# Kernel optimization log

Measured on AMD Instinct MI355X. Metric: run time of the kernel, lower is better.

The kernel has to match this reference:

```python
import jax, jax.numpy as jnp
import numpy as np
from functools import partial

I, H, O = 7, 64, 3  # input_size, hidden_layer_size, output_size
B, T = 512, 2048


def _lstm_scan(x, W_ih, W_hh, b_ih, b_hh, reverse):
    """Single-direction LSTM over [B,T,I]; returns hidden states [T,B,H]
    aligned to input time order (PyTorch gate order: i, f, g, o)."""
    Bsz = x.shape[0]
    Hh = W_hh.shape[1]
    # precompute input projections for all timesteps: [B,T,4H] -> [T,B,4H]
    xp = jnp.einsum('bti,gi->btg', x, W_ih) + b_ih + b_hh
    xp = jnp.swapaxes(xp, 0, 1)

    def step(carry, xt):
        h, c = carry
        gates = xt + h @ W_hh.T                      # [B,4H]
        i, f, g, o = jnp.split(gates, 4, axis=-1)
        i = jax.nn.sigmoid(i)
        f = jax.nn.sigmoid(f)
        g = jnp.tanh(g)
        o = jax.nn.sigmoid(o)
        c = f * c + i * g
        h = o * jnp.tanh(c)
        return (h, c), h

    h0 = jnp.zeros((Bsz, Hh), dtype=x.dtype)
    c0 = jnp.zeros((Bsz, Hh), dtype=x.dtype)
    (_, _), hs = jax.lax.scan(step, (h0, c0), xp, reverse=reverse)
    return hs  # [T,B,H], time-aligned


def setup_inputs() -> dict:
    key = jax.random.key(0)
    ks = jax.random.split(key, 12)
    s = 0.1  # ~ 1/sqrt(H) init scale
    return {
        'input_seq': jax.random.normal(ks[0], (B, T, I), dtype=jnp.float32),
        'W_ih_f': jax.random.normal(ks[1], (4 * H, I), dtype=jnp.float32) * s,
        'W_hh_f': jax.random.normal(ks[2], (4 * H, H), dtype=jnp.float32) * s,
        'b_ih_f': jax.random.normal(ks[3], (4 * H,), dtype=jnp.float32) * s,
        'b_hh_f': jax.random.normal(ks[4], (4 * H,), dtype=jnp.float32) * s,
        'W_ih_b': jax.random.normal(ks[5], (4 * H, I), dtype=jnp.float32) * s,
        'W_hh_b': jax.random.normal(ks[6], (4 * H, H), dtype=jnp.float32) * s,
        'b_ih_b': jax.random.normal(ks[7], (4 * H,), dtype=jnp.float32) * s,
        'b_hh_b': jax.random.normal(ks[8], (4 * H,), dtype=jnp.float32) * s,
        'W_lin': jax.random.normal(ks[9], (O, 2 * H), dtype=jnp.float32) * s,
        'b_lin': jax.random.normal(ks[10], (O,), dtype=jnp.float32) * s,
    }


def reference(input_seq, W_ih_f, W_hh_f, b_ih_f, b_hh_f,
              W_ih_b, W_hh_b, b_ih_b, b_hh_b, W_lin, b_lin):
    # forward direction: hidden at last timestep = hs_f[-1]
    hs_f = _lstm_scan(input_seq, W_ih_f, W_hh_f, b_ih_f, b_hh_f, reverse=False)
    # backward direction: scan reversed in time, outputs time-aligned, so
    # the value at t=T-1 is hs_b[-1] (the reverse LSTM's first computed step)
    hs_b = _lstm_scan(input_seq, W_ih_b, W_hh_b, b_ih_b, b_hh_b, reverse=True)
    last = jnp.concatenate([hs_f[-1], hs_b[-1]], axis=-1)  # [B, 2H]
    return last @ W_lin.T + b_lin  # [B, O]
```

## Files before the change

### kernel.cpp

```cpp
#include <hip/hip_runtime.h>
#include <hip/hip_bf16.h>

#define TT 2048
#define BB 512
#define HH 64
#define L2E 1.44269504088896340736f

typedef _Float16 h2 __attribute__((ext_vector_type(2)));

__device__ __forceinline__ float frcp(float x){ return __builtin_amdgcn_rcpf(x); }
__device__ __forceinline__ float fexp2(float x){ return __builtin_amdgcn_exp2f(x); }
__device__ __forceinline__ float fsig(float a){ return frcp(1.0f + __expf(-a)); }
__device__ __forceinline__ float ftanh(float a){ return 1.0f - 2.0f*frcp(__expf(2.0f*a)+1.0f); }
__device__ __forceinline__ h2 pk16(float lo, float hi){
  return __builtin_bit_cast(h2, __builtin_amdgcn_cvt_pkrtz(lo, hi));
}

__global__ void __launch_bounds__(64)
__attribute__((amdgpu_waves_per_eu(1, 1)))
lstm_fwd_kernel(
    const float* __restrict__ x, const float* __restrict__ Wih,
    const float* __restrict__ Whh, const float* __restrict__ bih,
    const float* __restrict__ bhh, float* __restrict__ hout)
{
  const int b = blockIdx.x;
  const int l = threadIdx.x;

  __shared__ float xs[TT][8];
  __shared__ int4  hlds4[HH/8];

  const float* xr = x + (size_t)b*TT*7;

  #pragma unroll 1
  for (int it = 0; it < TT/64; ++it){
    const int t = it*64 + l;
    const float* p = xr + (size_t)t*7;
    float4* dst = reinterpret_cast<float4*>(&xs[t][0]);
    dst[0] = make_float4(p[0],p[1],p[2],p[3]);
    dst[1] = make_float4(p[4],p[5],p[6],0.0f);
  }

  int wb[4][32];
  #pragma unroll
  for (int q = 0; q < 4; q++){
    const float sq = (q==2) ? (-2.0f*L2E) : (-L2E);
    const float4* wr = reinterpret_cast<const float4*>(Whh + (size_t)(q*HH + l)*HH);
    #pragma unroll
    for (int k = 0; k < 16; k++){
      float4 a = wr[k];
      h2 p0 = pk16(a.x*sq, a.y*sq);
      h2 p1 = pk16(a.z*sq, a.w*sq);
      wb[q][2*k+0] = __builtin_bit_cast(int, p0);
      wb[q][2*k+1] = __builtin_bit_cast(int, p1);
      asm volatile("" : "+v"(wb[q][2*k+0]), "+v"(wb[q][2*k+1]));
    }
    __builtin_amdgcn_sched_barrier(0);
  }

  int wi16[4][4];
  float bias[4];
  #pragma unroll
  for (int q = 0; q < 4; q++){
    const float sq = (q==2) ? (-2.0f*L2E) : (-L2E);
    const int g = q*HH + l;
    wi16[q][0] = __builtin_bit_cast(int, pk16(Wih[g*7+0]*sq, Wih[g*7+1]*sq));
    wi16[q][1] = __builtin_bit_cast(int, pk16(Wih[g*7+2]*sq, Wih[g*7+3]*sq));
    wi16[q][2] = __builtin_bit_cast(int, pk16(Wih[g*7+4]*sq, Wih[g*7+5]*sq));
    wi16[q][3] = __builtin_bit_cast(int, pk16(Wih[g*7+6]*sq, 0.0f));
    asm volatile("" : "+v"(wi16[q][0]), "+v"(wi16[q][1]),
                       "+v"(wi16[q][2]), "+v"(wi16[q][3]));
    bias[q] = (bih[g] + bhh[g])*sq;
    asm volatile("" : "+v"(bias[q]));
    __builtin_amdgcn_sched_barrier(0);
  }

  if (l < HH/8) hlds4[l] = int4{0,0,0,0};

  float h = 0.0f, c = 0.0f;

  int hw[32];
  #pragma unroll
  for (int i = 0; i < 8; i++){
    int4 v = hlds4[i];
    hw[4*i+0]=v.x; hw[4*i+1]=v.y; hw[4*i+2]=v.z; hw[4*i+3]=v.w;
  }

  #pragma unroll 1
  for (int t = 0; t < TT; ++t){
    const float4 xa = *reinterpret_cast<const float4*>(&xs[t][0]);
    const float4 xb = *reinterpret_cast<const float4*>(&xs[t][4]);
    const h2 xp0 = pk16(xa.x, xa.y);
    const h2 xp1 = pk16(xa.z, xa.w);
    const h2 xp2 = pk16(xb.x, xb.y);
    const h2 xp3 = pk16(xb.z, xb.w);

    float a0 = bias[0], a1 = bias[1], a2 = bias[2], a3 = bias[3];

    #pragma unroll
    for (int k = 0; k < 32; k++){
      const h2 hh = __builtin_bit_cast(h2, hw[k]);
      a0 = __builtin_amdgcn_fdot2(__builtin_bit_cast(h2, wb[0][k]), hh, a0, false);
      a1 = __builtin_amdgcn_fdot2(__builtin_bit_cast(h2, wb[1][k]), hh, a1, false);
      a2 = __builtin_amdgcn_fdot2(__builtin_bit_cast(h2, wb[2][k]), hh, a2, false);
      a3 = __builtin_amdgcn_fdot2(__builtin_bit_cast(h2, wb[3][k]), hh, a3, false);
    }
    #pragma unroll
    for (int p = 0; p < 4; p++){
      const h2 xp = (p==0)?xp0:(p==1)?xp1:(p==2)?xp2:xp3;
      a0 = __builtin_amdgcn_fdot2(__builtin_bit_cast(h2, wi16[0][p]), xp, a0, false);
      a1 = __builtin_amdgcn_fdot2(__builtin_bit_cast(h2, wi16[1][p]), xp, a1, false);
      a2 = __builtin_amdgcn_fdot2(__builtin_bit_cast(h2, wi16[2][p]), xp, a2, false);
      a3 = __builtin_amdgcn_fdot2(__builtin_bit_cast(h2, wi16[3][p]), xp, a3, false);
    }

    const float e0 = fexp2(a0);
    const float e1 = fexp2(a1);
    const float e2 = fexp2(a2);
    const float e3 = fexp2(a3);
    const float iv = frcp(1.0f + e0);
    const float fv = frcp(1.0f + e1);
    const float gv = 2.0f*frcp(1.0f + e2) - 1.0f;
    const float ov = frcp(1.0f + e3);

    c = fv*c + iv*gv;
    const float r  = frcp(1.0f + fexp2(c*(-2.0f*L2E)));
    h = 2.0f*ov*r - ov;

    reinterpret_cast<unsigned short*>(hlds4)[l] =
        __builtin_bit_cast(unsigned short, (_Float16)h);
    #pragma unroll
    for (int i = 0; i < 8; i++){
      int4 v = hlds4[i];
      hw[4*i+0]=v.x; hw[4*i+1]=v.y; hw[4*i+2]=v.z; hw[4*i+3]=v.w;
    }
  }
  hout[b*HH + l] = h;
}

__global__ __launch_bounds__(64, 1) void lstm_bwd_lin_kernel(
    const float* __restrict__ x,   const float* __restrict__ Wib,
    const float* __restrict__ bib, const float* __restrict__ bhb,
    const float* __restrict__ Wlin,const float* __restrict__ blin,
    const float* __restrict__ hf,  float* __restrict__ out)
{
  const int b = blockIdx.x;
  const int j = threadIdx.x;
  const float* xt = x + ((size_t)b*TT + (TT-1))*7;
  float xv[7];
  #pragma unroll
  for (int k = 0; k < 7; k++) xv[k] = xt[k];

  float g4[4];
  #pragma unroll
  for (int qq = 0; qq < 4; qq++){
    const int g = qq*HH + j;
    float a = bib[g] + bhb[g];
    #pragma unroll
    for (int k = 0; k < 7; k++) a += xv[k]*Wib[g*7+k];
    g4[qq] = a;
  }
  const float iv = fsig(g4[0]);
  const float gv = ftanh(g4[2]);
  const float ov = fsig(g4[3]);
  const float cc = iv*gv;
  const float hb = ov*ftanh(cc);
  const float hfv = hf[b*HH + j];

  float s[3];
  #pragma unroll
  for (int o = 0; o < 3; o++)
    s[o] = hfv*Wlin[o*128 + j] + hb*Wlin[o*128 + 64 + j];

  #pragma unroll
  for (int o = 0; o < 3; o++){
    float v = s[o];
    #pragma unroll
    for (int m = 32; m >= 1; m >>= 1) v += __shfl_xor(v, m, 64);
    s[o] = v;
  }
  if (j == 0){
    out[b*3+0] = s[0] + blin[0];
    out[b*3+1] = s[1] + blin[1];
    out[b*3+2] = s[2] + blin[2];
  }
}

extern "C" void kernel_launch(void* const* d_in, const int* in_sizes, int n_in,
                              void* d_out, int out_size, void* d_ws, size_t ws_size,
                              hipStream_t stream)
{
  const float* x    = (const float*)d_in[0];
  const float* Wihf = (const float*)d_in[1];
  const float* Whhf = (const float*)d_in[2];
  const float* bihf = (const float*)d_in[3];
  const float* bhhf = (const float*)d_in[4];
  const float* Wihb = (const float*)d_in[5];
  const float* bibb = (const float*)d_in[7];
  const float* bhbb = (const float*)d_in[8];
  const float* Wlin = (const float*)d_in[9];
  const float* blin = (const float*)d_in[10];
  float* out = (float*)d_out;
  float* hf  = (float*)d_ws;

  lstm_fwd_kernel<<<BB, 64, 0, stream>>>(x, Wihf, Whhf, bihf, bhhf, hf);
  lstm_bwd_lin_kernel<<<BB, 64, 0, stream>>>(x, Wihb, bibb, bhbb, Wlin, blin, hf, out);
}
```

Before: 826.2 us.

## Move g/o recurrent weights to LDS and allow two waves per EU

Keeps the i and f gate recurrent weights in registers and moves the g and o gate weights (fp16-packed) into shared memory, reloading them from LDS every timestep. This cuts VGPR use so the waves_per_eu hint can rise to 2, letting two blocks share an EU to hide the serial recurrence latency. x is also pre-packed to fp16 in LDS, so the per-step conversions disappear. The cost is 16 extra 128-bit LDS reads per step per lane, and LDS use grows to about 48KB per block, which may limit how many blocks fit per CU.

```diff
diff --git a/kernel.cpp b/kernel.cpp
--- a/kernel.cpp
+++ b/kernel.cpp
@@ -15,9 +15,13 @@
 __device__ __forceinline__ h2 pk16(float lo, float hi){
   return __builtin_bit_cast(h2, __builtin_amdgcn_cvt_pkrtz(lo, hi));
 }
+__device__ __forceinline__ float dot2(int w, int hp, float acc){
+  return __builtin_amdgcn_fdot2(__builtin_bit_cast(h2, w),
+                                __builtin_bit_cast(h2, hp), acc, false);
+}
 
 __global__ void __launch_bounds__(64)
-__attribute__((amdgpu_waves_per_eu(1, 1)))
+__attribute__((amdgpu_waves_per_eu(1, 2)))
 lstm_fwd_kernel(
     const float* __restrict__ x, const float* __restrict__ Wih,
     const float* __restrict__ Whh, const float* __restrict__ bih,
@@ -26,8 +30,9 @@
   const int b = blockIdx.x;
   const int l = threadIdx.x;
 
-  __shared__ float xs[TT][8];
-  __shared__ int4  hlds4[HH/8];
+  __shared__ int4 xsf4[TT];
+  __shared__ int4 wgo[2][8][HH];
+  __shared__ int4 hlds4[HH/8];
 
   const float* xr = x + (size_t)b*TT*7;
 
@@ -35,24 +40,49 @@
   for (int it = 0; it < TT/64; ++it){
     const int t = it*64 + l;
     const float* p = xr + (size_t)t*7;
-    float4* dst = reinterpret_cast<float4*>(&xs[t][0]);
-    dst[0] = make_float4(p[0],p[1],p[2],p[3]);
-    dst[1] = make_float4(p[4],p[5],p[6],0.0f);
-  }
-
-  int wb[4][32];
-  #pragma unroll
-  for (int q = 0; q < 4; q++){
-    const float sq = (q==2) ? (-2.0f*L2E) : (-L2E);
+    int4 v;
+    v.x = __builtin_bit_cast(int, pk16(p[0], p[1]));
+    v.y = __builtin_bit_cast(int, pk16(p[2], p[3]));
+    v.z = __builtin_bit_cast(int, pk16(p[4], p[5]));
+    v.w = __builtin_bit_cast(int, pk16(p[6], 0.0f));
+    xsf4[t] = v;
+  }
+
+  #pragma unroll
+  for (int g = 0; g < 2; ++g){
+    const int q = 2 + g;
+    const float sq = (q == 2) ? (-2.0f*L2E) : (-L2E);
     const float4* wr = reinterpret_cast<const float4*>(Whh + (size_t)(q*HH + l)*HH);
     #pragma unroll
+    for (int kb = 0; kb < 8; ++kb){
+      float4 a = wr[2*kb], b4 = wr[2*kb+1];
+      int4 v;
+      v.x = __builtin_bit_cast(int, pk16(a.x*sq,  a.y*sq));
+      v.y = __builtin_bit_cast(int, pk16(a.z*sq,  a.w*sq));
+      v.z = __builtin_bit_cast(int, pk16(b4.x*sq, b4.y*sq));
+      v.w = __builtin_bit_cast(int, pk16(b4.z*sq, b4.w*sq));
+      wgo[g][kb][l] = v;
+    }
+  }
+
+  int wbi[32], wbf[32];
+  {
+    const float4* wri = reinterpret_cast<const float4*>(Whh + (size_t)(0*HH + l)*HH);
+    const float4* wrf = reinterpret_cast<const float4*>(Whh + (size_t)(1*HH + l)*HH);
+    #pragma unroll
     for (int k = 0; k < 16; k++){
-      float4 a = wr[k];
-      h2 p0 = pk16(a.x*sq, a.y*sq);
-      h2 p1 = pk16(a.z*sq, a.w*sq);
-      wb[q][2*k+0] = __builtin_bit_cast(int, p0);
-      wb[q][2*k+1] = __builtin_bit_cast(int, p1);
-      asm volatile("" : "+v"(wb[q][2*k+0]), "+v"(wb[q][2*k+1]));
+      float4 a = wri[k];
+      wbi[2*k+0] = __builtin_bit_cast(int, pk16(a.x*(-L2E), a.y*(-L2E)));
+      wbi[2*k+1] = __builtin_bit_cast(int, pk16(a.z*(-L2E), a.w*(-L2E)));
+      asm volatile("" : "+v"(wbi[2*k+0]), "+v"(wbi[2*k+1]));
+    }
+    __builtin_amdgcn_sched_barrier(0);
+    #pragma unroll
+    for (int k = 0; k < 16; k++){
+      float4 a = wrf[k];
+      wbf[2*k+0] = __builtin_bit_cast(int, pk16(a.x*(-L2E), a.y*(-L2E)));
+      wbf[2*k+1] = __builtin_bit_cast(int, pk16(a.z*(-L2E), a.w*(-L2E)));
+      asm volatile("" : "+v"(wbf[2*k+0]), "+v"(wbf[2*k+1]));
     }
     __builtin_amdgcn_sched_barrier(0);
   }
@@ -67,11 +97,7 @@
     wi16[q][1] = __builtin_bit_cast(int, pk16(Wih[g*7+2]*sq, Wih[g*7+3]*sq));
     wi16[q][2] = __builtin_bit_cast(int, pk16(Wih[g*7+4]*sq, Wih[g*7+5]*sq));
     wi16[q][3] = __builtin_bit_cast(int, pk16(Wih[g*7+6]*sq, 0.0f));
-    asm volatile("" : "+v"(wi16[q][0]), "+v"(wi16[q][1]),
-                       "+v"(wi16[q][2]), "+v"(wi16[q][3]));
     bias[q] = (bih[g] + bhh[g])*sq;
-    asm volatile("" : "+v"(bias[q]));
-    __builtin_amdgcn_sched_barrier(0);
   }
 
   if (l < HH/8) hlds4[l] = int4{0,0,0,0};
@@ -87,31 +113,48 @@
 
   #pragma unroll 1
   for (int t = 0; t < TT; ++t){
-    const float4 xa = *reinterpret_cast<const float4*>(&xs[t][0]);
-    const float4 xb = *reinterpret_cast<const float4*>(&xs[t][4]);
-    const h2 xp0 = pk16(xa.x, xa.y);
-    const h2 xp1 = pk16(xa.z, xa.w);
-    const h2 xp2 = pk16(xb.x, xb.y);
-    const h2 xp3 = pk16(xb.z, xb.w);
+    const int4 xv = xsf4[t];
+
+    int4 g0 = wgo[0][0][l], g1 = wgo[0][1][l], g2 = wgo[0][2][l], g3 = wgo[0][3][l];
+    int4 g4 = wgo[0][4][l], g5 = wgo[0][5][l], g6 = wgo[0][6][l], g7 = wgo[0][7][l];
 
     float a0 = bias[0], a1 = bias[1], a2 = bias[2], a3 = bias[3];
 
     #pragma unroll
     for (int k = 0; k < 32; k++){
-      const h2 hh = __builtin_bit_cast(h2, hw[k]);
-      a0 = __builtin_amdgcn_fdot2(__builtin_bit_cast(h2, wb[0][k]), hh, a0, false);
-      a1 = __builtin_amdgcn_fdot2(__builtin_bit_cast(h2, wb[1][k]), hh, a1, false);
-      a2 = __builtin_amdgcn_fdot2(__builtin_bit_cast(h2, wb[2][k]), hh, a2, false);
-      a3 = __builtin_amdgcn_fdot2(__builtin_bit_cast(h2, wb[3][k]), hh, a3, false);
-    }
-    #pragma unroll
-    for (int p = 0; p < 4; p++){
-      const h2 xp = (p==0)?xp0:(p==1)?xp1:(p==2)?xp2:xp3;
-      a0 = __builtin_amdgcn_fdot2(__builtin_bit_cast(h2, wi16[0][p]), xp, a0, false);
-      a1 = __builtin_amdgcn_fdot2(__builtin_bit_cast(h2, wi16[1][p]), xp, a1, false);
-      a2 = __builtin_amdgcn_fdot2(__builtin_bit_cast(h2, wi16[2][p]), xp, a2, false);
-      a3 = __builtin_amdgcn_fdot2(__builtin_bit_cast(h2, wi16[3][p]), xp, a3, false);
-    }
+      a0 = dot2(wbi[k], hw[k], a0);
+      a1 = dot2(wbf[k], hw[k], a1);
+    }
+
+    int4 o0 = wgo[1][0][l], o1 = wgo[1][1][l], o2 = wgo[1][2][l], o3 = wgo[1][3][l];
+    int4 o4 = wgo[1][4][l], o5 = wgo[1][5][l], o6 = wgo[1][6][l], o7 = wgo[1][7][l];
+
+    #define GDOT(gg, kb) \
+      a2 = dot2((gg).x, hw[4*(kb)+0], a2); \
+      a2 = dot2((gg).y, hw[4*(kb)+1], a2); \
+      a2 = dot2((gg).z, hw[4*(kb)+2], a2); \
+      a2 = dot2((gg).w, hw[4*(kb)+3], a2);
+    GDOT(g0,0) GDOT(g1,1) GDOT(g2,2) GDOT(g3,3)
+    GDOT(g4,4) GDOT(g5,5) GDOT(g6,6) GDOT(g7,7)
+    #undef GDOT
+
+    #define ODOT(oo, kb) \
+      a3 = dot2((oo).x, hw[4*(kb)+0], a3); \
+      a3 = dot2((oo).y, hw[4*(kb)+1], a3); \
+      a3 = dot2((oo).z, hw[4*(kb)+2], a3); \
+      a3 = dot2((oo).w, hw[4*(kb)+3], a3);
+    ODOT(o0,0) ODOT(o1,1) ODOT(o2,2) ODOT(o3,3)
+    ODOT(o4,4) ODOT(o5,5) ODOT(o6,6) ODOT(o7,7)
+    #undef ODOT
+
+    a0 = dot2(wi16[0][0], xv.x, a0); a0 = dot2(wi16[0][1], xv.y, a0);
+    a0 = dot2(wi16[0][2], xv.z, a0); a0 = dot2(wi16[0][3], xv.w, a0);
+    a1 = dot2(wi16[1][0], xv.x, a1); a1 = dot2(wi16[1][1], xv.y, a1);
+    a1 = dot2(wi16[1][2], xv.z, a1); a1 = dot2(wi16[1][3], xv.w, a1);
+    a2 = dot2(wi16[2][0], xv.x, a2); a2 = dot2(wi16[2][1], xv.y, a2);
+    a2 = dot2(wi16[2][2], xv.z, a2); a2 = dot2(wi16[2][3], xv.w, a2);
+    a3 = dot2(wi16[3][0], xv.x, a3); a3 = dot2(wi16[3][1], xv.y, a3);
+    a3 = dot2(wi16[3][2], xv.z, a3); a3 = dot2(wi16[3][3], xv.w, a3);
 
     const float e0 = fexp2(a0);
     const float e1 = fexp2(a1);
@@ -123,7 +166,7 @@
     const float ov = frcp(1.0f + e3);
 
     c = fv*c + iv*gv;
-    const float r  = frcp(1.0f + fexp2(c*(-2.0f*L2E)));
+    const float r = frcp(1.0f + fexp2(c*(-2.0f*L2E)));
     h = 2.0f*ov*r - ov;
 
     reinterpret_cast<unsigned short*>(hlds4)[l] =
```

Measured after the change: 796.7 us. 3.6% less time.

## Process two batch rows per wavefront with W_hh staged in LDS

Applied to the files above, without the earlier changes.

Each 64-lane block now runs two independent batch sequences, interleaving their recurrences so one sequence's dot products and transcendentals can hide the other's latency. The recurrent weights move from registers into LDS and are reread every step, and x is pre-packed to fp16 in LDS. This halves the grid to 256 blocks, which is about one wave per CU on a 256-CU part, and adds per-step LDS weight traffic in exchange for more instruction-level parallelism per wave.

```diff
diff --git a/kernel.cpp b/kernel.cpp
--- a/kernel.cpp
+++ b/kernel.cpp
@@ -14,6 +14,13 @@
 __device__ __forceinline__ float ftanh(float a){ return 1.0f - 2.0f*frcp(__expf(2.0f*a)+1.0f); }
 __device__ __forceinline__ h2 pk16(float lo, float hi){
   return __builtin_bit_cast(h2, __builtin_amdgcn_cvt_pkrtz(lo, hi));
+}
+__device__ __forceinline__ int pk16i(float lo, float hi){
+  return __builtin_bit_cast(int, pk16(lo, hi));
+}
+__device__ __forceinline__ float dot2(int w, int hp, float acc){
+  return __builtin_amdgcn_fdot2(__builtin_bit_cast(h2, w),
+                                __builtin_bit_cast(h2, hp), acc, false);
 }
 
 __global__ void __launch_bounds__(64)
@@ -23,38 +30,43 @@
     const float* __restrict__ Whh, const float* __restrict__ bih,
     const float* __restrict__ bhh, float* __restrict__ hout)
 {
-  const int b = blockIdx.x;
-  const int l = threadIdx.x;
-
-  __shared__ float xs[TT][8];
-  __shared__ int4  hlds4[HH/8];
-
-  const float* xr = x + (size_t)b*TT*7;
+  const int b0 = blockIdx.x * 2;
+  const int l  = threadIdx.x;
+
+  __shared__ int4 xsf[2][TT];
+  __shared__ int4 wlds[4][8][HH];
+  __shared__ int4 hlds[2][HH/8];
 
   #pragma unroll 1
-  for (int it = 0; it < TT/64; ++it){
-    const int t = it*64 + l;
-    const float* p = xr + (size_t)t*7;
-    float4* dst = reinterpret_cast<float4*>(&xs[t][0]);
-    dst[0] = make_float4(p[0],p[1],p[2],p[3]);
-    dst[1] = make_float4(p[4],p[5],p[6],0.0f);
-  }
-
-  int wb[4][32];
-  #pragma unroll
-  for (int q = 0; q < 4; q++){
-    const float sq = (q==2) ? (-2.0f*L2E) : (-L2E);
+  for (int r = 0; r < 2; ++r){
+    const float* xr = x + (size_t)(b0 + r)*TT*7;
+    #pragma unroll 1
+    for (int it = 0; it < TT/64; ++it){
+      const int t = it*64 + l;
+      const float* p = xr + (size_t)t*7;
+      int4 v;
+      v.x = pk16i(p[0], p[1]);
+      v.y = pk16i(p[2], p[3]);
+      v.z = pk16i(p[4], p[5]);
+      v.w = pk16i(p[6], 0.0f);
+      xsf[r][t] = v;
+    }
+  }
+
+  #pragma unroll
+  for (int q = 0; q < 4; ++q){
+    const float sq = (q == 2) ? (-2.0f*L2E) : (-L2E);
     const float4* wr = reinterpret_cast<const float4*>(Whh + (size_t)(q*HH + l)*HH);
     #pragma unroll
-    for (int k = 0; k < 16; k++){
-      float4 a = wr[k];
-      h2 p0 = pk16(a.x*sq, a.y*sq);
-      h2 p1 = pk16(a.z*sq, a.w*sq);
-      wb[q][2*k+0] = __builtin_bit_cast(int, p0);
-      wb[q][2*k+1] = __builtin_bit_cast(int, p1);
-      asm volatile("" : "+v"(wb[q][2*k+0]), "+v"(wb[q][2*k+1]));
-    }
-    __builtin_amdgcn_sched_barrier(0);
+    for (int kb = 0; kb < 8; ++kb){
+      float4 a = wr[2*kb], b4 = wr[2*kb+1];
+      int4 v;
+      v.x = pk16i(a.x*sq,  a.y*sq);
+      v.y = pk16i(a.z*sq,  a.w*sq);
+      v.z = pk16i(b4.x*sq, b4.y*sq);
+      v.w = pk16i(b4.z*sq, b4.w*sq);
+      wlds[q][kb][l] = v;
+    }
   }
 
   int wi16[4][4];
@@ -63,78 +75,117 @@
   for (int q = 0; q < 4; q++){
     const float sq = (q==2) ? (-2.0f*L2E) : (-L2E);
     const int g = q*HH + l;
-    wi16[q][0] = __builtin_bit_cast(int, pk16(Wih[g*7+0]*sq, Wih[g*7+1]*sq));
-    wi16[q][1] = __builtin_bit_cast(int, pk16(Wih[g*7+2]*sq, Wih[g*7+3]*sq));
-    wi16[q][2] = __builtin_bit_cast(int, pk16(Wih[g*7+4]*sq, Wih[g*7+5]*sq));
-    wi16[q][3] = __builtin_bit_cast(int, pk16(Wih[g*7+6]*sq, 0.0f));
-    asm volatile("" : "+v"(wi16[q][0]), "+v"(wi16[q][1]),
-                       "+v"(wi16[q][2]), "+v"(wi16[q][3]));
+    wi16[q][0] = pk16i(Wih[g*7+0]*sq, Wih[g*7+1]*sq);
+    wi16[q][1] = pk16i(Wih[g*7+2]*sq, Wih[g*7+3]*sq);
+    wi16[q][2] = pk16i(Wih[g*7+4]*sq, Wih[g*7+5]*sq);
+    wi16[q][3] = pk16i(Wih[g*7+6]*sq, 0.0f);
     bias[q] = (bih[g] + bhh[g])*sq;
-    asm volatile("" : "+v"(bias[q]));
-    __builtin_amdgcn_sched_barrier(0);
-  }
-
-  if (l < HH/8) hlds4[l] = int4{0,0,0,0};
-
-  float h = 0.0f, c = 0.0f;
-
-  int hw[32];
+  }
+
+  {
+    int4* hf = &hlds[0][0];
+    if (l < 16) hf[l] = int4{0,0,0,0};
+  }
+
+  float h0 = 0.0f, c0 = 0.0f, h1 = 0.0f, c1 = 0.0f;
+
+  int hw0[32], hw1[32];
   #pragma unroll
   for (int i = 0; i < 8; i++){
-    int4 v = hlds4[i];
-    hw[4*i+0]=v.x; hw[4*i+1]=v.y; hw[4*i+2]=v.z; hw[4*i+3]=v.w;
-  }
+    int4 v = hlds[0][i];
+    hw0[4*i+0]=v.x; hw0[4*i+1]=v.y; hw0[4*i+2]=v.z; hw0[4*i+3]=v.w;
+  }
+  #pragma unroll
+  for (int i = 0; i < 8; i++){
+    int4 v = hlds[1][i];
+    hw1[4*i+0]=v.x; hw1[4*i+1]=v.y; hw1[4*i+2]=v.z; hw1[4*i+3]=v.w;
+  }
+  int4 xv0 = xsf[0][0];
+  int4 xv1 = xsf[1][0];
 
   #pragma unroll 1
   for (int t = 0; t < TT; ++t){
-    const float4 xa = *reinterpret_cast<const float4*>(&xs[t][0]);
-    const float4 xb = *reinterpret_cast<const float4*>(&xs[t][4]);
-    const h2 xp0 = pk16(xa.x, xa.y);
-    const h2 xp1 = pk16(xa.z, xa.w);
-    const h2 xp2 = pk16(xb.x, xb.y);
-    const h2 xp3 = pk16(xb.z, xb.w);
-
-    float a0 = bias[0], a1 = bias[1], a2 = bias[2], a3 = bias[3];
-
-    #pragma unroll
-    for (int k = 0; k < 32; k++){
-      const h2 hh = __builtin_bit_cast(h2, hw[k]);
-      a0 = __builtin_amdgcn_fdot2(__builtin_bit_cast(h2, wb[0][k]), hh, a0, false);
-      a1 = __builtin_amdgcn_fdot2(__builtin_bit_cast(h2, wb[1][k]), hh, a1, false);
-      a2 = __builtin_amdgcn_fdot2(__builtin_bit_cast(h2, wb[2][k]), hh, a2, false);
-      a3 = __builtin_amdgcn_fdot2(__builtin_bit_cast(h2, wb[3][k]), hh, a3, false);
-    }
-    #pragma unroll
-    for (int p = 0; p < 4; p++){
-      const h2 xp = (p==0)?xp0:(p==1)?xp1:(p==2)?xp2:xp3;
-      a0 = __builtin_amdgcn_fdot2(__builtin_bit_cast(h2, wi16[0][p]), xp, a0, false);
-      a1 = __builtin_amdgcn_fdot2(__builtin_bit_cast(h2, wi16[1][p]), xp, a1, false);
-      a2 = __builtin_amdgcn_fdot2(__builtin_bit_cast(h2, wi16[2][p]), xp, a2, false);
-      a3 = __builtin_amdgcn_fdot2(__builtin_bit_cast(h2, wi16[3][p]), xp, a3, false);
-    }
-
-    const float e0 = fexp2(a0);
-    const float e1 = fexp2(a1);
-    const float e2 = fexp2(a2);
-    const float e3 = fexp2(a3);
-    const float iv = frcp(1.0f + e0);
-    const float fv = frcp(1.0f + e1);
-    const float gv = 2.0f*frcp(1.0f + e2) - 1.0f;
-    const float ov = frcp(1.0f + e3);
-
-    c = fv*c + iv*gv;
-    const float r  = frcp(1.0f + fexp2(c*(-2.0f*L2E)));
-    h = 2.0f*ov*r - ov;
-
-    reinterpret_cast<unsigned short*>(hlds4)[l] =
-        __builtin_bit_cast(unsigned short, (_Float16)h);
-    #pragma unroll
-    for (int i = 0; i < 8; i++){
-      int4 v = hlds4[i];
-      hw[4*i+0]=v.x; hw[4*i+1]=v.y; hw[4*i+2]=v.z; hw[4*i+3]=v.w;
-    }
-  }
-  hout[b*HH + l] = h;
+    float a00 = bias[0], a01 = bias[1], a02 = bias[2], a03 = bias[3];
+    float a10 = bias[0], a11 = bias[1], a12 = bias[2], a13 = bias[3];
+
+    a00 = dot2(wi16[0][0], xv0.x, a00); a00 = dot2(wi16[0][1], xv0.y, a00);
+    a00 = dot2(wi16[0][2], xv0.z, a00); a00 = dot2(wi16[0][3], xv0.w, a00);
+    a01 = dot2(wi16[1][0], xv0.x, a01); a01 = dot2(wi16[1][1], xv0.y, a01);
+    a01 = dot2(wi16[1][2], xv0.z, a01); a01 = dot2(wi16[1][3], xv0.w, a01);
+    a02 = dot2(wi16[2][0], xv0.x, a02); a02 = dot2(wi16[2][1], xv0.y, a02);
+    a02 = dot2(wi16[2][2], xv0.z, a02); a02 = dot2(wi16[2][3], xv0.w, a02);
+    a03 = dot2(wi16[3][0], xv0.x, a03); a03 = dot2(wi16[3][1], xv0.y, a03);
+    a03 = dot2(wi16[3][2], xv0.z, a03); a03 = dot2(wi16[3][3], xv0.w, a03);
+
+    a10 = dot2(wi16[0][0], xv1.x, a10); a10 = dot2(wi16[0][1], xv1.y, a10);
+    a10 = dot2(wi16[0][2], xv1.z, a10); a10 = dot2(wi16[0][3], xv1.w, a10);
+    a11 = dot2(wi16[1][0], xv1.x, a11); a11 = dot2(wi16[1][1], xv1.y, a11);
+    a11 = dot2(wi16[1][2], xv1.z, a11); a11 = dot2(wi16[1][3], xv1.w, a11);
+    a12 = dot2(wi16[2][0], xv1.x, a12); a12 = dot2(wi16[2][1], xv1.y, a12);
+    a12 = dot2(wi16[2][2], xv1.z, a12); a12 = dot2(wi16[2][3], xv1.w, a12);
+    a13 = dot2(wi16[3][0], xv1.x, a13); a13 = dot2(wi16[3][1], xv1.y, a13);
+    a13 = dot2(wi16[3][2], xv1.z, a13); a13 = dot2(wi16[3][3], xv1.w, a13);
+
+    #pragma unroll
+    for (int q = 0; q < 4; ++q){
+      int4 w0 = wlds[q][0][l], w1 = wlds[q][1][l], w2 = wlds[q][2][l], w3 = wlds[q][3][l];
+      int4 w4 = wlds[q][4][l], w5 = wlds[q][5][l], w6 = wlds[q][6][l], w7 = wlds[q][7][l];
+      float s0, s1;
+      s0 = (q==0)?a00:(q==1)?a01:(q==2)?a02:a03;
+      s1 = (q==0)?a10:(q==1)?a11:(q==2)?a12:a13;
+      #define QD(w_, kb) \
+        s0 = dot2((w_).x, hw0[4*(kb)+0], s0); s0 = dot2((w_).y, hw0[4*(kb)+1], s0); \
+        s0 = dot2((w_).z, hw0[4*(kb)+2], s0); s0 = dot2((w_).w, hw0[4*(kb)+3], s0); \
+        s1 = dot2((w_).x, hw1[4*(kb)+0], s1); s1 = dot2((w_).y, hw1[4*(kb)+1], s1); \
+        s1 = dot2((w_).z, hw1[4*(kb)+2], s1); s1 = dot2((w_).w, hw1[4*(kb)+3], s1);
+      QD(w0,0) QD(w1,1) QD(w2,2) QD(w3,3) QD(w4,4) QD(w5,5) QD(w6,6) QD(w7,7)
+      #undef QD
+      if (q==0){ a00=s0; a10=s1; } else if (q==1){ a01=s0; a11=s1; }
+      else if (q==2){ a02=s0; a12=s1; } else { a03=s0; a13=s1; }
+    }
+
+    {
+      const float e0 = fexp2(a00), e1 = fexp2(a01), e2 = fexp2(a02), e3 = fexp2(a03);
+      const float iv = frcp(1.0f + e0);
+      const float fv = frcp(1.0f + e1);
+      const float gv = 2.0f*frcp(1.0f + e2) - 1.0f;
+      const float ov = frcp(1.0f + e3);
+      c0 = fv*c0 + iv*gv;
+      const float r = frcp(1.0f + fexp2(c0*(-2.0f*L2E)));
+      h0 = 2.0f*ov*r - ov;
+      reinterpret_cast<unsigned short*>(&hlds[0][0])[l] =
+          __builtin_bit_cast(unsigned short, (_Float16)h0);
+      #pragma unroll
+      for (int i = 0; i < 8; i++){
+        int4 v = hlds[0][i];
+        hw0[4*i+0]=v.x; hw0[4*i+1]=v.y; hw0[4*i+2]=v.z; hw0[4*i+3]=v.w;
+      }
+    }
+
+    {
+      const float e0 = fexp2(a10), e1 = fexp2(a11), e2 = fexp2(a12), e3 = fexp2(a13);
+      const float iv = frcp(1.0f + e0);
+      const float fv = frcp(1.0f + e1);
+      const float gv = 2.0f*frcp(1.0f + e2) - 1.0f;
+      const float ov = frcp(1.0f + e3);
+      c1 = fv*c1 + iv*gv;
+      const float r = frcp(1.0f + fexp2(c1*(-2.0f*L2E)));
+      h1 = 2.0f*ov*r - ov;
+      reinterpret_cast<unsigned short*>(&hlds[1][0])[l] =
+          __builtin_bit_cast(unsigned short, (_Float16)h1);
+      #pragma unroll
+      for (int i = 0; i < 8; i++){
+        int4 v = hlds[1][i];
+        hw1[4*i+0]=v.x; hw1[4*i+1]=v.y; hw1[4*i+2]=v.z; hw1[4*i+3]=v.w;
+      }
+    }
+
+    const int tn = (t+1) & (TT-1);
+    xv0 = xsf[0][tn];
+    xv1 = xsf[1][tn];
+  }
+  hout[(b0+0)*HH + l] = h0;
+  hout[(b0+1)*HH + l] = h1;
 }
 
 __global__ __launch_bounds__(64, 1) void lstm_bwd_lin_kernel(
@@ -202,6 +253,6 @@
   float* out = (float*)d_out;
   float* hf  = (float*)d_ws;
 
-  lstm_fwd_kernel<<<BB, 64, 0, stream>>>(x, Wihf, Whhf, bihf, bhhf, hf);
+  lstm_fwd_kernel<<<BB/2, 64, 0, stream>>>(x, Wihf, Whhf, bihf, bhhf, hf);
   lstm_bwd_lin_kernel<<<BB, 64, 0, stream>>>(x, Wihb, bibb, bhbb, Wlin, blin, hf, out);
 }
```

Result: slower. 1.755 ms (+112.4%).
